# Kernel tuning notes

Measured on AMD Instinct MI355X. Metric: run time of the kernel, lower is better.

## Reference

```python
import jax, jax.numpy as jnp
import numpy as np

RMS_EPS = 1e-6

def setup_inputs() -> dict:
    key = jax.random.key(0)
    ks = jax.random.split(key, 4)
    G, S, F, H, E = 4, 2048, 2048, 4096, 8
    return {
        "x": jax.random.normal(ks[0], (G, S, F), dtype=jnp.float32),
        "w_router": jax.random.normal(ks[1], (F, E), dtype=jnp.float32) * 0.02,
        "w_gating": jax.random.normal(ks[2], (E, 2, H, F), dtype=jnp.float32) * 0.02,
        "w_linear": jax.random.normal(ks[3], (E, H, F), dtype=jnp.float32) * 0.02,
        "per_expert_scale": jnp.ones((E,), dtype=jnp.float32),
        "router_scale": jnp.ones((F,), dtype=jnp.float32),
        "top_k": 2,
    }

def reference(x, w_router, w_gating, w_linear, per_expert_scale, router_scale, top_k):
    G, S, F = x.shape
    E = w_router.shape[1]
    H = w_linear.shape[1]
    k = top_k

    # ---- router (RMSNorm without scale, then scaled projection) ----
    var = jnp.mean(jnp.square(x), axis=-1, keepdims=True)
    router_input = x * jax.lax.rsqrt(var + RMS_EPS)
    root_size = jax.lax.rsqrt(jnp.array(F, dtype=router_input.dtype))
    router_input = router_input * root_size * router_scale.astype(router_input.dtype)
    logits = jnp.einsum('gsd,de->gse', router_input, w_router).astype(jnp.float32)
    router_probs = jax.nn.softmax(logits, axis=-1)          # (G,S,E)
    _, choices = jax.lax.approx_max_k(logits, k=k)          # (G,S,k)

    # renormalization over selected experts
    indicator = jax.nn.one_hot(choices, E, dtype=router_probs.dtype).sum(axis=-2)  # (G,S,E)
    renorm = jnp.sum(indicator * router_probs, axis=-1, keepdims=True)
    renorm = jnp.where(renorm > 0.0, renorm, 1.0)
    weights = router_probs / renorm                          # (G,S,E)

    # ---- dispatch: sort token copies by expert ----
    B = G * S
    xf = x.reshape(B, F)
    cf = choices.reshape(-1)                                 # (B*k,)
    order = jnp.argsort(cf)
    rev = jnp.argsort(order)
    idx = jnp.repeat(jnp.arange(B), k)[order]
    sorted_xs = xf[idx, :]                                   # (B*k, F)
    oh = jax.nn.one_hot(choices, E, dtype=jnp.int32)         # (G,S,k,E)
    tokens_per_expert = jnp.sum(oh, axis=(0, 1, 2))          # (E,)
    combine = (oh.astype(jnp.float32) * weights[:, :, None, :]).sum(-1).astype(weights.dtype)  # (G,S,k)

    # ---- grouped GEMM GLU FFN via ragged_dot ----
    w_gate = jnp.transpose(w_gating, (0, 3, 1, 2)).reshape(E, F, 2 * H)
    gate_out = jax.lax.ragged_dot(sorted_xs, w_gate, group_sizes=tokens_per_expert)  # (B*k, 2H)
    gate_out = gate_out.reshape(gate_out.shape[0], 2, H)
    activation = jax.nn.gelu(gate_out[:, 0, :]) * gate_out[:, 1, :]
    expert_outputs = jax.lax.ragged_dot(activation, w_linear, group_sizes=tokens_per_expert)  # (B*k, F)
    expert_idx = jnp.repeat(jnp.arange(E), tokens_per_expert, total_repeat_length=expert_outputs.shape[0])
    expert_outputs = expert_outputs * per_expert_scale.astype(expert_outputs.dtype)[expert_idx, None]

    # ---- collect and combine ----
    out = expert_outputs[rev].reshape(G, S, k, F)
    out = jnp.einsum('gskd,gsk->gsd', out, combine.astype(out.dtype))
    return out
```

## Files before the change

kernel.cpp:

```cpp
#include <hip/hip_runtime.h>
#include <stdint.h>

#define F_DIM 2048
#define H_DIM 4096
#define E_NUM 8
#define B_TOK 8192
#define T_ROWS 16384
#define T_PAD  16512
#define NMB_MAX 72
#define BK 64
#define BM 256
#define BN 256

typedef __attribute__((ext_vector_type(8))) short bf16x8;
typedef __attribute__((ext_vector_type(4))) float f32x4;

__device__ __forceinline__ unsigned short f2bf(float f) {
  union { float f; unsigned u; } v; v.f = f;
  unsigned u = v.u;
  unsigned r = u + 0x7fffu + ((u >> 16) & 1u);
  return (unsigned short)(r >> 16);
}
__device__ __forceinline__ float bf2f(unsigned short u) {
  union { unsigned u; float f; } v; v.u = ((unsigned)u) << 16;
  return v.f;
}
__device__ __forceinline__ float gelu_tanh(float x) {
  float z = 0.7978845608028654f * (x + 0.044715f * x * x * x);
  float t = 1.0f - 2.0f / (__expf(2.0f * z) + 1.0f);
  return 0.5f * x * (1.0f + t);
}
__device__ __forceinline__ void gload16(const void* g, void* l) {
  __builtin_amdgcn_global_load_lds(
      (const __attribute__((address_space(1))) void*)g,
      (__attribute__((address_space(3))) void*)l, 16, 0, 0);
}

__global__ __launch_bounds__(256) void k_convert(const float* __restrict__ src,
                                                 unsigned short* __restrict__ dst,
                                                 long n4) {
  long i = (long)blockIdx.x * blockDim.x + threadIdx.x;
  long stride = (long)gridDim.x * blockDim.x;
  for (; i < n4; i += stride) {
    float4 v = ((const float4*)src)[i];
    ushort4 o;
    o.x = f2bf(v.x); o.y = f2bf(v.y); o.z = f2bf(v.z); o.w = f2bf(v.w);
    ((ushort4*)dst)[i] = o;
  }
}

__global__ __launch_bounds__(256) void k_router(const float* __restrict__ x,
                                                const float* __restrict__ wr,
                                                const float* __restrict__ rscale,
                                                const float* __restrict__ pes,
                                                int* __restrict__ counts,
                                                int* __restrict__ meta_e,
                                                float* __restrict__ meta_w) {
  int t = blockIdx.x;
  int tid = threadIdx.x;
  const float4* x4 = (const float4*)(x + (long)t * F_DIM);
  float4 v0 = x4[tid], v1 = x4[tid + 256];
  const float4* s4 = (const float4*)rscale;
  float4 s0 = s4[tid], s1 = s4[tid + 256];

  __shared__ float red[4];
  __shared__ float lg[4][8];

  float ss = v0.x * v0.x + v0.y * v0.y + v0.z * v0.z + v0.w * v0.w +
             v1.x * v1.x + v1.y * v1.y + v1.z * v1.z + v1.w * v1.w;
  for (int o = 32; o >= 1; o >>= 1) ss += __shfl_down(ss, o, 64);
  if ((tid & 63) == 0) red[tid >> 6] = ss;
  __syncthreads();
  float sumsq = red[0] + red[1] + red[2] + red[3];
  float scale = rsqrtf(sumsq * (1.0f / F_DIM) + 1e-6f) * rsqrtf((float)F_DIM);

  float acc[8];
#pragma unroll
  for (int e = 0; e < 8; e++) acc[e] = 0.f;
#pragma unroll
  for (int j = 0; j < 4; j++) {
    float u = ((const float*)&v0)[j] * ((const float*)&s0)[j];
    const float4* wrow = (const float4*)(wr + (long)(4 * tid + j) * 8);
    float4 wa = wrow[0], wb = wrow[1];
    acc[0] += u * wa.x; acc[1] += u * wa.y; acc[2] += u * wa.z; acc[3] += u * wa.w;
    acc[4] += u * wb.x; acc[5] += u * wb.y; acc[6] += u * wb.z; acc[7] += u * wb.w;
  }
#pragma unroll
  for (int j = 0; j < 4; j++) {
    float u = ((const float*)&v1)[j] * ((const float*)&s1)[j];
    const float4* wrow = (const float4*)(wr + (long)(4 * (tid + 256) + j) * 8);
    float4 wa = wrow[0], wb = wrow[1];
    acc[0] += u * wa.x; acc[1] += u * wa.y; acc[2] += u * wa.z; acc[3] += u * wa.w;
    acc[4] += u * wb.x; acc[5] += u * wb.y; acc[6] += u * wb.z; acc[7] += u * wb.w;
  }
#pragma unroll
  for (int e = 0; e < 8; e++) {
    float a = acc[e];
    for (int o = 32; o >= 1; o >>= 1) a += __shfl_down(a, o, 64);
    if ((tid & 63) == 0) lg[tid >> 6][e] = a;
  }
  __syncthreads();
  if (tid == 0) {
    float l[8];
#pragma unroll
    for (int e = 0; e < 8; e++)
      l[e] = (lg[0][e] + lg[1][e] + lg[2][e] + lg[3][e]) * scale;
    int e0 = 0;
    for (int e = 1; e < 8; e++) if (l[e] > l[e0]) e0 = e;
    int e1 = (e0 == 0) ? 1 : 0;
    for (int e = 0; e < 8; e++) if (e != e0 && l[e] > l[e1]) e1 = e;
    float p1 = __expf(l[e1] - l[e0]);
    float inv = 1.0f / (1.0f + p1);
    meta_e[2 * t] = e0; meta_e[2 * t + 1] = e1;
    meta_w[2 * t] = inv * pes[e0];
    meta_w[2 * t + 1] = p1 * inv * pes[e1];
    atomicAdd(&counts[e0], 1);
    atomicAdd(&counts[e1], 1);
  }
}

__global__ void k_sched(const int* __restrict__ counts, int* __restrict__ segoff,
                        int* __restrict__ nblocks, int4* __restrict__ sched) {
  if (threadIdx.x == 0 && blockIdx.x == 0) {
    int off = 0, nb = 0;
    for (int e = 0; e < 8; e++) {
      segoff[e] = off;
      int c = counts[e];
      int end = off + c;
      for (int i = 0; i < c; i += BM) {
        sched[nb].x = off + i; sched[nb].y = end; sched[nb].z = e; nb++;
      }
      off = end;
    }
    segoff[8] = off;
    *nblocks = nb;
    for (int b = nb; b < NMB_MAX; b++) { sched[b].x = 0; sched[b].y = 0; sched[b].z = 0; }
  }
}

__global__ __launch_bounds__(256) void k_scatter(const int* __restrict__ meta_e,
                                                 const int* __restrict__ segoff,
                                                 int* __restrict__ fills,
                                                 int* __restrict__ meta_pos,
                                                 int* __restrict__ tok_of_row) {
  int t = blockIdx.x * blockDim.x + threadIdx.x;
  if (t >= B_TOK) return;
#pragma unroll
  for (int s = 0; s < 2; s++) {
    int e = meta_e[2 * t + s];
    int pos = segoff[e] + atomicAdd(&fills[e], 1);
    meta_pos[2 * t + s] = pos;
    tok_of_row[pos] = t;
  }
}

__global__ __launch_bounds__(256) void k_gather(const float* __restrict__ x,
                                                const int* __restrict__ tok_of_row,
                                                unsigned short* __restrict__ sx) {
  int r = blockIdx.x;
  int tid = threadIdx.x;
  unsigned short* dst = sx + (long)r * F_DIM;
  if (r < T_ROWS) {
    const float4* src = (const float4*)(x + (long)tok_of_row[r] * F_DIM);
    for (int i = tid; i < F_DIM / 4; i += 256) {
      float4 v = src[i];
      ushort4 o;
      o.x = f2bf(v.x); o.y = f2bf(v.y); o.z = f2bf(v.z); o.w = f2bf(v.w);
      ((ushort4*)dst)[i] = o;
    }
  } else {
    ushort4 z = make_ushort4(0, 0, 0, 0);
    for (int i = tid; i < F_DIM / 4; i += 256) ((ushort4*)dst)[i] = z;
  }
}


#define DSA(MH) \
  _Pragma("unroll") for (int mt = 0; mt < 4; mt++) \
  _Pragma("unroll") for (int ks = 0; ks < 2; ks++) { \
    int r_ = wm * 128 + (MH) * 64 + mt * 16 + lrow; \
    aR[mt * 2 + ks] = *(const bf16x8*)&sA[cur][r_ * BK + ((((ks << 2) + q) ^ (r_ & 7)) << 3)]; \
  }

#define DSB(NH) \
  _Pragma("unroll") for (int nt = 0; nt < 2; nt++) \
  _Pragma("unroll") for (int ks = 0; ks < 2; ks++) { \
    int r_ = wn * 64 + (NH) * 32 + nt * 16 + lrow; \
    bR[nt * 2 + ks] = *(const bf16x8*)&sB[cur][r_ * BK + ((((ks << 2) + q) ^ (r_ & 7)) << 3)]; \
  }

#define MMA(MH, NH) \
  _Pragma("unroll") for (int mt = 0; mt < 4; mt++) \
  _Pragma("unroll") for (int nt = 0; nt < 2; nt++) \
  _Pragma("unroll") for (int ks = 0; ks < 2; ks++) \
    acc[(MH) * 4 + mt][(NH) * 2 + nt] = __builtin_amdgcn_mfma_f32_16x16x32_bf16( \
        aR[mt * 2 + ks], bR[nt * 2 + ks], acc[(MH) * 4 + mt][(NH) * 2 + nt], 0, 0, 0);

#define PHASE_PRE \
  asm volatile("s_barrier" ::: "memory"); \
  asm volatile("s_waitcnt lgkmcnt(0)" ::: "memory"); \
  __builtin_amdgcn_sched_barrier(0); \
  __builtin_amdgcn_s_setprio(1);

#define PHASE_POST \
  __builtin_amdgcn_s_setprio(0); \
  __builtin_amdgcn_sched_barrier(0); \
  asm volatile("s_barrier" ::: "memory");

#define ITER_TOP(VMC) \
  asm volatile("s_waitcnt vmcnt(" #VMC ")" ::: "memory"); \
  __builtin_amdgcn_sched_barrier(0); \
  asm volatile("s_barrier" ::: "memory"); \
  __builtin_amdgcn_sched_barrier(0);

__global__ __launch_bounds__(512, 2) void k_gemm_gate(
    const unsigned short* __restrict__ sx,
    const unsigned short* __restrict__ wg,
    const int4* __restrict__ sched, const int* __restrict__ nblocks,
    unsigned short* __restrict__ act)
{
  int mb = blockIdx.y;
  if (mb >= *nblocks) return;
  int4 sc = sched[mb];
  int row0 = sc.x, row_end = sc.y, e = sc.z;
  int h0 = blockIdx.x * 128;

  __shared__ __align__(16) unsigned short sA[2][BM * BK];
  __shared__ __align__(16) unsigned short sB[2][BM * BK];

  int tid = threadIdx.x, lane = tid & 63, w = tid >> 6;
  int wm = w >> 2, wn = w & 3;
  int lrow = lane & 15, q = lane >> 4;
  int srow8 = lane >> 3;
  int scol = ((lane & 7) ^ srow8) << 3;

  const unsigned short* B0 = wg + ((long)e * 2 * H_DIM + h0) * F_DIM;
  const unsigned short* B1 = wg + ((long)e * 2 * H_DIM + H_DIM + h0) * F_DIM;

  f32x4 acc[8][4];
  f32x4 z4 = {0.f, 0.f, 0.f, 0.f};
#pragma unroll
  for (int i_ = 0; i_ < 8; i_++)
#pragma unroll
    for (int j_ = 0; j_ < 4; j_++) acc[i_][j_] = z4;
  bf16x8 aR[8], bR[4];

#define STAGE_G1(T) { \
    int k0_ = (T) * BK; \
    unsigned short* dA = &sA[(T) & 1][0]; \
    unsigned short* dB = &sB[(T) & 1][0]; \
    _Pragma("unroll") for (int i = 0; i < 4; i++) { \
      int c = w * 4 + i; \
      int rA_ = row0 + 8 * c + srow8; rA_ = rA_ < T_PAD - 1 ? rA_ : T_PAD - 1; \
      gload16(sx + (long)rA_ * F_DIM + k0_ + scol, (char*)dA + c * 1024 + lane * 16); \
      int rB_ = 8 * c + srow8; \
      const unsigned short* bb = (((c >> 1) & 1) ? B1 : B0); \
      int hr_ = ((rB_ >> 5) << 4) + (rB_ & 15); \
      gload16(bb + (long)hr_ * F_DIM + k0_ + scol, (char*)dB + c * 1024 + lane * 16); \
    } }

  const int NT = F_DIM / BK;
  STAGE_G1(0);
  for (int t = 0; t < NT; ++t) {
    int cur = t & 1;
    if (t + 1 < NT) {
      STAGE_G1(t + 1);
      ITER_TOP(8)
    } else {
      ITER_TOP(0)
    }
    DSA(0); DSB(0); PHASE_PRE; MMA(0, 0); PHASE_POST;
    DSB(1);         PHASE_PRE; MMA(0, 1); PHASE_POST;
    DSA(1);         PHASE_PRE; MMA(1, 1); PHASE_POST;
    DSB(0);         PHASE_PRE; MMA(1, 0); PHASE_POST;
  }
#undef STAGE_G1

  int lr4 = q * 4;
#pragma unroll
  for (int mt = 0; mt < 8; mt++) {
#pragma unroll
    for (int hf = 0; hf < 2; hf++) {
      f32x4 g0 = acc[mt][hf * 2], g1 = acc[mt][hf * 2 + 1];
      int h = h0 + (wn * 2 + hf) * 16 + lrow;
      long mbase = row0 + wm * 128 + mt * 16 + lr4;
#pragma unroll
      for (int r = 0; r < 4; r++) {
        long m = mbase + r;
        if (m < row_end)
          act[m * H_DIM + h] = f2bf(gelu_tanh(g0[r]) * g1[r]);
      }
    }
  }
}

__global__ __launch_bounds__(256) void k_transpose(const float* __restrict__ wl,
                                                   unsigned short* __restrict__ wlt) {
  __shared__ float t[64 * 65];
  int e = blockIdx.z;
  int h0 = blockIdx.y * 64, f0 = blockIdx.x * 64;
  int tx = threadIdx.x & 63, ty = threadIdx.x >> 6;
  const float* src = wl + ((long)e * H_DIM + h0) * F_DIM + f0;
#pragma unroll
  for (int r = 0; r < 16; r++) {
    int hl = r * 4 + ty;
    t[hl * 65 + tx] = src[(long)hl * F_DIM + tx];
  }
  __syncthreads();
  unsigned short* dst = wlt + ((long)e * F_DIM + f0) * H_DIM + h0;
#pragma unroll
  for (int r = 0; r < 16; r++) {
    int fl = r * 4 + ty;
    dst[(long)fl * H_DIM + tx] = f2bf(t[tx * 65 + fl]);
  }
}

__global__ __launch_bounds__(512, 2) void k_gemm_out(
    const unsigned short* __restrict__ act,
    const unsigned short* __restrict__ wlt,
    const int4* __restrict__ sched, const int* __restrict__ nblocks,
    unsigned short* __restrict__ eout)
{
  int mb = blockIdx.y;
  if (mb >= *nblocks) return;
  int4 sc = sched[mb];
  int row0 = sc.x, row_end = sc.y, e = sc.z;
  int n0 = blockIdx.x * BN;

  __shared__ __align__(16) unsigned short sA[2][BM * BK];
  __shared__ __align__(16) unsigned short sB[2][BM * BK];

  int tid = threadIdx.x, lane = tid & 63, w = tid >> 6;
  int wm = w >> 2, wn = w & 3;
  int lrow = lane & 15, q = lane >> 4;
  int srow8 = lane >> 3;
  int scol = ((lane & 7) ^ srow8) << 3;

  const unsigned short* Bb = wlt + ((long)e * F_DIM + n0) * H_DIM;

  f32x4 acc[8][4];
  f32x4 z4 = {0.f, 0.f, 0.f, 0.f};
#pragma unroll
  for (int i_ = 0; i_ < 8; i_++)
#pragma unroll
    for (int j_ = 0; j_ < 4; j_++) acc[i_][j_] = z4;
  bf16x8 aR[8], bR[4];

#define STAGE_G2(T) { \
    int k0_ = (T) * BK; \
    unsigned short* dA = &sA[(T) & 1][0]; \
    unsigned short* dB = &sB[(T) & 1][0]; \
    _Pragma("unroll") for (int i = 0; i < 4; i++) { \
      int c = w * 4 + i; \
      int rA_ = row0 + 8 * c + srow8; rA_ = rA_ < T_PAD - 1 ? rA_ : T_PAD - 1; \
      gload16(act + (long)rA_ * H_DIM + k0_ + scol, (char*)dA + c * 1024 + lane * 16); \
      int rB_ = 8 * c + srow8; \
      gload16(Bb + (long)rB_ * H_DIM + k0_ + scol, (char*)dB + c * 1024 + lane * 16); \
    } }

  const int NT = H_DIM / BK;
  STAGE_G2(0);
  for (int t = 0; t < NT; ++t) {
    int cur = t & 1;
    if (t + 1 < NT) {
      STAGE_G2(t + 1);
      ITER_TOP(8)
    } else {
      ITER_TOP(0)
    }
    DSA(0); DSB(0); PHASE_PRE; MMA(0, 0); PHASE_POST;
    DSB(1);         PHASE_PRE; MMA(0, 1); PHASE_POST;
    DSA(1);         PHASE_PRE; MMA(1, 1); PHASE_POST;
    DSB(0);         PHASE_PRE; MMA(1, 0); PHASE_POST;
  }
#undef STAGE_G2

  int lr4 = q * 4;
#pragma unroll
  for (int mt = 0; mt < 8; mt++) {
#pragma unroll
    for (int j = 0; j < 4; j++) {
      f32x4 c4 = acc[mt][j];
      int f = n0 + wn * 64 + j * 16 + lrow;
      long mbase = row0 + wm * 128 + mt * 16 + lr4;
#pragma unroll
      for (int r = 0; r < 4; r++) {
        long m = mbase + r;
        if (m < row_end)
          eout[m * F_DIM + f] = f2bf(c4[r]);
      }
    }
  }
}

__global__ __launch_bounds__(256) void k_combine(const unsigned short* __restrict__ eout,
                                                 const int* __restrict__ meta_pos,
                                                 const float* __restrict__ meta_w,
                                                 float* __restrict__ out) {
  int t = blockIdx.x;
  int tid = threadIdx.x;
  int p0 = meta_pos[2 * t], p1 = meta_pos[2 * t + 1];
  float w0 = meta_w[2 * t], w1 = meta_w[2 * t + 1];
  const ushort4* r0 = (const ushort4*)(eout + (long)p0 * F_DIM);
  const ushort4* r1 = (const ushort4*)(eout + (long)p1 * F_DIM);
  float4* o = (float4*)(out + (long)t * F_DIM);
  for (int i = tid; i < F_DIM / 4; i += 256) {
    ushort4 a = r0[i], b = r1[i];
    float4 v;
    v.x = w0 * bf2f(a.x) + w1 * bf2f(b.x);
    v.y = w0 * bf2f(a.y) + w1 * bf2f(b.y);
    v.z = w0 * bf2f(a.z) + w1 * bf2f(b.z);
    v.w = w0 * bf2f(a.w) + w1 * bf2f(b.w);
    o[i] = v;
  }
}

#define WG_OFF   0L
#define SX_OFF   268435456L
#define ACT_OFF  (268435456L + 67633152L)
#define CTRL_OFF (ACT_OFF + 135266304L)

extern "C" void kernel_launch(void* const* d_in, const int* in_sizes, int n_in,
                              void* d_out, int out_size, void* d_ws, size_t ws_size,
                              hipStream_t stream) {
  const float* x    = (const float*)d_in[0];
  const float* wr   = (const float*)d_in[1];
  const float* wgat = (const float*)d_in[2];
  const float* wlin = (const float*)d_in[3];
  const float* pes  = (const float*)d_in[4];
  const float* rsc  = (const float*)d_in[5];
  float* out = (float*)d_out;

  char* ws = (char*)d_ws;
  unsigned short* wg_bf = (unsigned short*)(ws + WG_OFF);
  unsigned short* wlt   = (unsigned short*)(ws + WG_OFF);
  unsigned short* sx    = (unsigned short*)(ws + SX_OFF);
  unsigned short* eout  = (unsigned short*)(ws + SX_OFF);
  unsigned short* act   = (unsigned short*)(ws + ACT_OFF);
  char* ctrl = ws + CTRL_OFF;
  int*   counts   = (int*)(ctrl + 0);
  int*   fills    = (int*)(ctrl + 32);
  int*   segoff   = (int*)(ctrl + 64);
  int*   nblocks  = (int*)(ctrl + 128);
  int4*  sched    = (int4*)(ctrl + 256);
  int*   meta_e   = (int*)(ctrl + 4096);
  int*   meta_pos = (int*)(ctrl + 4096 + 65536);
  float* meta_w   = (float*)(ctrl + 4096 + 131072);
  int*   tok_of_row = (int*)(ctrl + 4096 + 196608);

  hipMemsetAsync(ctrl, 0, 64, stream);

  k_convert<<<16384, 256, 0, stream>>>(wgat, wg_bf, (long)E_NUM * 2 * H_DIM * F_DIM / 4);
  k_router<<<B_TOK, 256, 0, stream>>>(x, wr, rsc, pes, counts, meta_e, meta_w);
  k_sched<<<1, 64, 0, stream>>>(counts, segoff, nblocks, sched);
  k_scatter<<<B_TOK / 256, 256, 0, stream>>>(meta_e, segoff, fills, meta_pos, tok_of_row);
  k_gather<<<T_PAD, 256, 0, stream>>>(x, tok_of_row, sx);
  k_gemm_gate<<<dim3(2 * H_DIM / BN, NMB_MAX), 512, 0, stream>>>(sx, wg_bf, sched, nblocks, act);
  k_transpose<<<dim3(F_DIM / 64, H_DIM / 64, E_NUM), 256, 0, stream>>>(wlin, wlt);
  k_gemm_out<<<dim3(F_DIM / BN, NMB_MAX), 512, 0, stream>>>(act, wlt, sched, nblocks, eout);
  k_combine<<<B_TOK, 256, 0, stream>>>(eout, meta_pos, meta_w, out);
}
```

Before: 2.626 ms.

## Split A/B staging, double-buffer B fragments, and remap workgroups across XCDs

The two grouped GEMM kernels now issue the next tile's A loads at the top of each iteration and defer the B loads until after the first MMA phase. B fragments are held in two register sets so the last phase reuses bR0 instead of reloading it from LDS. Workgroup IDs are remapped so that consecutive blocks on the same XCD share weight or activation tiles, aiming at better L2 reuse. The gload16 destination also drops the per-lane offset, which only works if gload16 adds the lane offset itself (an LDS-direct load). The trade-offs are more register pressure and a riskier ordering of waits and barriers.

```diff
diff --git a/kernel.cpp b/kernel.cpp
--- a/kernel.cpp
+++ b/kernel.cpp
@@ -182,19 +182,19 @@
     aR[mt * 2 + ks] = *(const bf16x8*)&sA[cur][r_ * BK + ((((ks << 2) + q) ^ (r_ & 7)) << 3)]; \
   }
 
-#define DSB(NH) \
+#define DSB(DST, NH) \
   _Pragma("unroll") for (int nt = 0; nt < 2; nt++) \
   _Pragma("unroll") for (int ks = 0; ks < 2; ks++) { \
     int r_ = wn * 64 + (NH) * 32 + nt * 16 + lrow; \
-    bR[nt * 2 + ks] = *(const bf16x8*)&sB[cur][r_ * BK + ((((ks << 2) + q) ^ (r_ & 7)) << 3)]; \
-  }
-
-#define MMA(MH, NH) \
+    DST[nt * 2 + ks] = *(const bf16x8*)&sB[cur][r_ * BK + ((((ks << 2) + q) ^ (r_ & 7)) << 3)]; \
+  }
+
+#define MMA(MH, BR, NH) \
   _Pragma("unroll") for (int mt = 0; mt < 4; mt++) \
   _Pragma("unroll") for (int nt = 0; nt < 2; nt++) \
   _Pragma("unroll") for (int ks = 0; ks < 2; ks++) \
     acc[(MH) * 4 + mt][(NH) * 2 + nt] = __builtin_amdgcn_mfma_f32_16x16x32_bf16( \
-        aR[mt * 2 + ks], bR[nt * 2 + ks], acc[(MH) * 4 + mt][(NH) * 2 + nt], 0, 0, 0);
+        aR[mt * 2 + ks], BR[nt * 2 + ks], acc[(MH) * 4 + mt][(NH) * 2 + nt], 0, 0, 0);
 
 #define PHASE_PRE \
   asm volatile("s_barrier" ::: "memory"); \
@@ -207,11 +207,20 @@
   __builtin_amdgcn_sched_barrier(0); \
   asm volatile("s_barrier" ::: "memory");
 
-#define ITER_TOP(VMC) \
+#define ITOP(VMC) \
   asm volatile("s_waitcnt vmcnt(" #VMC ")" ::: "memory"); \
   __builtin_amdgcn_sched_barrier(0); \
   asm volatile("s_barrier" ::: "memory"); \
   __builtin_amdgcn_sched_barrier(0);
+
+#define PH1_MID \
+  asm volatile("s_waitcnt lgkmcnt(0)" ::: "memory"); \
+  __builtin_amdgcn_sched_barrier(0); \
+  __builtin_amdgcn_s_setprio(1);
+
+__device__ __forceinline__ int xcd_remap(int lin, int nwg) {
+  return (lin & 7) * (nwg >> 3) + (lin >> 3);
+}
 
 __global__ __launch_bounds__(512, 2) void k_gemm_gate(
     const unsigned short* __restrict__ sx,
@@ -219,11 +228,14 @@
     const int4* __restrict__ sched, const int* __restrict__ nblocks,
     unsigned short* __restrict__ act)
 {
-  int mb = blockIdx.y;
+  int lin = blockIdx.y * gridDim.x + blockIdx.x;
+  int logical = xcd_remap(lin, NMB_MAX * 32);
+  int mb = logical % NMB_MAX;
+  int nbk = logical / NMB_MAX;
   if (mb >= *nblocks) return;
   int4 sc = sched[mb];
   int row0 = sc.x, row_end = sc.y, e = sc.z;
-  int h0 = blockIdx.x * 128;
+  int h0 = nbk * 128;
 
   __shared__ __align__(16) unsigned short sA[2][BM * BK];
   __shared__ __align__(16) unsigned short sB[2][BM * BK];
@@ -243,38 +255,46 @@
   for (int i_ = 0; i_ < 8; i_++)
 #pragma unroll
     for (int j_ = 0; j_ < 4; j_++) acc[i_][j_] = z4;
-  bf16x8 aR[8], bR[4];
-
-#define STAGE_G1(T) { \
+  bf16x8 aR[8], bR0[4], bR1[4];
+
+#define STAGE_A1(T) { \
     int k0_ = (T) * BK; \
     unsigned short* dA = &sA[(T) & 1][0]; \
+    _Pragma("unroll") for (int i = 0; i < 4; i++) { \
+      int c = w * 4 + i; \
+      int rA_ = row0 + 8 * c + srow8; rA_ = rA_ < T_PAD - 1 ? rA_ : T_PAD - 1; \
+      gload16(sx + (long)rA_ * F_DIM + k0_ + scol, (char*)dA + c * 1024); \
+    } }
+#define STAGE_B1(T) { \
+    int k0_ = (T) * BK; \
     unsigned short* dB = &sB[(T) & 1][0]; \
     _Pragma("unroll") for (int i = 0; i < 4; i++) { \
       int c = w * 4 + i; \
-      int rA_ = row0 + 8 * c + srow8; rA_ = rA_ < T_PAD - 1 ? rA_ : T_PAD - 1; \
-      gload16(sx + (long)rA_ * F_DIM + k0_ + scol, (char*)dA + c * 1024 + lane * 16); \
       int rB_ = 8 * c + srow8; \
       const unsigned short* bb = (((c >> 1) & 1) ? B1 : B0); \
       int hr_ = ((rB_ >> 5) << 4) + (rB_ & 15); \
-      gload16(bb + (long)hr_ * F_DIM + k0_ + scol, (char*)dB + c * 1024 + lane * 16); \
+      gload16(bb + (long)hr_ * F_DIM + k0_ + scol, (char*)dB + c * 1024); \
     } }
 
   const int NT = F_DIM / BK;
-  STAGE_G1(0);
+  STAGE_A1(0); STAGE_B1(0);
   for (int t = 0; t < NT; ++t) {
     int cur = t & 1;
     if (t + 1 < NT) {
-      STAGE_G1(t + 1);
-      ITER_TOP(8)
+      STAGE_A1(t + 1);
+      ITOP(4)
     } else {
-      ITER_TOP(0)
-    }
-    DSA(0); DSB(0); PHASE_PRE; MMA(0, 0); PHASE_POST;
-    DSB(1);         PHASE_PRE; MMA(0, 1); PHASE_POST;
-    DSA(1);         PHASE_PRE; MMA(1, 1); PHASE_POST;
-    DSB(0);         PHASE_PRE; MMA(1, 0); PHASE_POST;
-  }
-#undef STAGE_G1
+      ITOP(0)
+    }
+    DSA(0); DSB(bR0, 0);
+    PH1_MID; MMA(0, bR0, 0); PHASE_POST;
+    if (t + 1 < NT) STAGE_B1(t + 1);
+    DSB(bR1, 1); PHASE_PRE; MMA(0, bR1, 1); PHASE_POST;
+    DSA(1);      PHASE_PRE; MMA(1, bR1, 1); PHASE_POST;
+                 PHASE_PRE; MMA(1, bR0, 0); PHASE_POST;
+  }
+#undef STAGE_A1
+#undef STAGE_B1
 
   int lr4 = q * 4;
 #pragma unroll
@@ -321,11 +341,14 @@
     const int4* __restrict__ sched, const int* __restrict__ nblocks,
     unsigned short* __restrict__ eout)
 {
-  int mb = blockIdx.y;
+  int lin = blockIdx.y * gridDim.x + blockIdx.x;
+  int logical = xcd_remap(lin, NMB_MAX * 8);
+  int nbk = logical % 8;
+  int mb = logical / 8;
   if (mb >= *nblocks) return;
   int4 sc = sched[mb];
   int row0 = sc.x, row_end = sc.y, e = sc.z;
-  int n0 = blockIdx.x * BN;
+  int n0 = nbk * BN;
 
   __shared__ __align__(16) unsigned short sA[2][BM * BK];
   __shared__ __align__(16) unsigned short sB[2][BM * BK];
@@ -344,36 +367,44 @@
   for (int i_ = 0; i_ < 8; i_++)
 #pragma unroll
     for (int j_ = 0; j_ < 4; j_++) acc[i_][j_] = z4;
-  bf16x8 aR[8], bR[4];
-
-#define STAGE_G2(T) { \
+  bf16x8 aR[8], bR0[4], bR1[4];
+
+#define STAGE_A2(T) { \
     int k0_ = (T) * BK; \
     unsigned short* dA = &sA[(T) & 1][0]; \
+    _Pragma("unroll") for (int i = 0; i < 4; i++) { \
+      int c = w * 4 + i; \
+      int rA_ = row0 + 8 * c + srow8; rA_ = rA_ < T_PAD - 1 ? rA_ : T_PAD - 1; \
+      gload16(act + (long)rA_ * H_DIM + k0_ + scol, (char*)dA + c * 1024); \
+    } }
+#define STAGE_B2(T) { \
+    int k0_ = (T) * BK; \
     unsigned short* dB = &sB[(T) & 1][0]; \
     _Pragma("unroll") for (int i = 0; i < 4; i++) { \
       int c = w * 4 + i; \
-      int rA_ = row0 + 8 * c + srow8; rA_ = rA_ < T_PAD - 1 ? rA_ : T_PAD - 1; \
-      gload16(act + (long)rA_ * H_DIM + k0_ + scol, (char*)dA + c * 1024 + lane * 16); \
       int rB_ = 8 * c + srow8; \
-      gload16(Bb + (long)rB_ * H_DIM + k0_ + scol, (char*)dB + c * 1024 + lane * 16); \
+      gload16(Bb + (long)rB_ * H_DIM + k0_ + scol, (char*)dB + c * 1024); \
     } }
 
   const int NT = H_DIM / BK;
-  STAGE_G2(0);
+  STAGE_A2(0); STAGE_B2(0);
   for (int t = 0; t < NT; ++t) {
     int cur = t & 1;
     if (t + 1 < NT) {
-      STAGE_G2(t + 1);
-      ITER_TOP(8)
+      STAGE_A2(t + 1);
+      ITOP(4)
     } else {
-      ITER_TOP(0)
-    }
-    DSA(0); DSB(0); PHASE_PRE; MMA(0, 0); PHASE_POST;
-    DSB(1);         PHASE_PRE; MMA(0, 1); PHASE_POST;
-    DSA(1);         PHASE_PRE; MMA(1, 1); PHASE_POST;
-    DSB(0);         PHASE_PRE; MMA(1, 0); PHASE_POST;
-  }
-#undef STAGE_G2
+      ITOP(0)
+    }
+    DSA(0); DSB(bR0, 0);
+    PH1_MID; MMA(0, bR0, 0); PHASE_POST;
+    if (t + 1 < NT) STAGE_B2(t + 1);
+    DSB(bR1, 1); PHASE_PRE; MMA(0, bR1, 1); PHASE_POST;
+    DSA(1);      PHASE_PRE; MMA(1, bR1, 1); PHASE_POST;
+                 PHASE_PRE; MMA(1, bR0, 0); PHASE_POST;
+  }
+#undef STAGE_A2
+#undef STAGE_B2
 
   int lr4 = q * 4;
 #pragma unroll
@@ -455,8 +486,8 @@
   k_sched<<<1, 64, 0, stream>>>(counts, segoff, nblocks, sched);
   k_scatter<<<B_TOK / 256, 256, 0, stream>>>(meta_e, segoff, fills, meta_pos, tok_of_row);
   k_gather<<<T_PAD, 256, 0, stream>>>(x, tok_of_row, sx);
-  k_gemm_gate<<<dim3(2 * H_DIM / BN, NMB_MAX), 512, 0, stream>>>(sx, wg_bf, sched, nblocks, act);
+  k_gemm_gate<<<dim3(NMB_MAX, 32), 512, 0, stream>>>(sx, wg_bf, sched, nblocks, act);
   k_transpose<<<dim3(F_DIM / 64, H_DIM / 64, E_NUM), 256, 0, stream>>>(wlin, wlt);
-  k_gemm_out<<<dim3(F_DIM / BN, NMB_MAX), 512, 0, stream>>>(act, wlt, sched, nblocks, eout);
+  k_gemm_out<<<dim3(NMB_MAX, 8), 512, 0, stream>>>(act, wlt, sched, nblocks, eout);
   k_combine<<<B_TOK, 256, 0, stream>>>(eout, meta_pos, meta_w, out);
 }
```

New measurement: 2.609 ms. Within noise of the previous version (-0.6%).
